# Kernel tuning notes

Measured on AMD Instinct MI355X. Metric: run time of the kernel, lower is better.

The kernel has to match this reference:

```python
import jax, jax.numpy as jnp
import numpy as np

N = 100000      # nodes
E = 1600000     # edges
F = 128         # num_node_features
H = 128         # hidden_channels
C = 10          # num_classes
R = 2           # num relations
G = 512         # num graphs in the batch


def setup_inputs() -> dict:
    key = jax.random.key(0)
    ks = jax.random.split(key, 16)
    s = 0.05
    x = jax.random.normal(ks[0], (N, F), dtype=jnp.float32)
    edge_index = jax.random.randint(ks[1], (2, E), 0, N, dtype=jnp.int64)
    edge_attr = jax.random.randint(ks[2], (E,), 0, R, dtype=jnp.int64)
    batch = jnp.sort(jax.random.randint(ks[3], (N,), 0, G, dtype=jnp.int64))
    W1 = jax.random.normal(ks[4], (R, F, H), dtype=jnp.float32) * s
    root1 = jax.random.normal(ks[5], (F, H), dtype=jnp.float32) * s
    b1 = jnp.zeros((H,), dtype=jnp.float32)
    W2 = jax.random.normal(ks[6], (R, H, H), dtype=jnp.float32) * s
    root2 = jax.random.normal(ks[7], (H, H), dtype=jnp.float32) * s
    b2 = jnp.zeros((H,), dtype=jnp.float32)
    W3 = jax.random.normal(ks[8], (R, H, H), dtype=jnp.float32) * s
    root3 = jax.random.normal(ks[9], (H, H), dtype=jnp.float32) * s
    b3 = jnp.zeros((H,), dtype=jnp.float32)
    lin_w = jax.random.normal(ks[10], (H, C), dtype=jnp.float32) * s
    lin_b = jnp.zeros((C,), dtype=jnp.float32)
    return dict(x=x, edge_index=edge_index, edge_attr=edge_attr, batch=batch,
                W1=W1, root1=root1, b1=b1, W2=W2, root2=root2, b2=b2,
                W3=W3, root3=root3, b3=b3, lin_w=lin_w, lin_b=lin_b)


def _rgcn_layer(x, src, dst, edge_type, W, root, b):
    # PyG RGCNConv: out = x @ root + b + sum_r mean_{edges of rel r -> i}(x_j @ W_r)
    n = x.shape[0]
    out = x @ root + b
    for r in range(R):
        h = x @ W[r]                               # [N, H] transform-then-gather
        w = (edge_type == r).astype(x.dtype)       # [E] relation mask
        num = jax.ops.segment_sum(h[src] * w[:, None], dst, num_segments=n)
        cnt = jax.ops.segment_sum(w, dst, num_segments=n)
        out = out + num / jnp.maximum(cnt, 1.0)[:, None]
    return out


def reference(x, edge_index, edge_attr, batch, W1, root1, b1, W2, root2, b2,
              W3, root3, b3, lin_w, lin_b):
    src, dst = edge_index[0], edge_index[1]
    h = jax.nn.relu(_rgcn_layer(x, src, dst, edge_attr, W1, root1, b1))
    h = jax.nn.relu(_rgcn_layer(h, src, dst, edge_attr, W2, root2, b2))
    h = jax.nn.relu(_rgcn_layer(h, src, dst, edge_attr, W3, root3, b3))
    # global mean pool over graphs
    psum = jax.ops.segment_sum(h, batch, num_segments=G)
    pcnt = jax.ops.segment_sum(jnp.ones((h.shape[0],), h.dtype), batch, num_segments=G)
    pooled = psum / jnp.maximum(pcnt, 1.0)[:, None]
    return pooled @ lin_w + lin_b
```

## Files before the change

kernel.cpp:

```cpp
#include <hip/hip_runtime.h>
#include <hip/hip_bf16.h>

#define Nn 100000
#define Ee 1600000
#define Ff 128
#define Hh 128
#define Cc 10
#define Gg 512

#define NBK 391
#define ABLK 4096
#define NABLK ((Ee + ABLK - 1) / ABLK)
#define BMAX 5376

typedef short bf16x8 __attribute__((ext_vector_type(8)));
typedef float f32x4 __attribute__((ext_vector_type(4)));
typedef float f32x2 __attribute__((ext_vector_type(2)));

__device__ __forceinline__ unsigned short f2bf(float f) {
    unsigned u = __float_as_uint(f);
    u += 0x7fffu + ((u >> 16) & 1u);
    return (unsigned short)(u >> 16);
}
__device__ __forceinline__ unsigned pk2(float a, float b) {
    return (unsigned)f2bf(a) | ((unsigned)f2bf(b) << 16);
}

__global__ __launch_bounds__(256) void cast_x(const float* __restrict__ x,
                                              uint2* __restrict__ xb) {
    int i = blockIdx.x * 256 + threadIdx.x;
    if (i >= Nn * Ff / 4) return;
    float4 v = ((const float4*)x)[i];
    uint2 o;
    o.x = pk2(v.x, v.y);
    o.y = pk2(v.z, v.w);
    xb[i] = o;
}

__global__ __launch_bounds__(256) void pack_w(const float* __restrict__ W1, const float* __restrict__ r1,
                                              const float* __restrict__ W2, const float* __restrict__ r2,
                                              const float* __restrict__ W3, const float* __restrict__ r3,
                                              unsigned short* __restrict__ wp) {
    int t = blockIdx.x * 256 + threadIdx.x;
    if (t >= 9 * 16384) return;
    int i = t & 7, l = (t >> 3) & 63, s = (t >> 9) & 3, c = (t >> 11) & 7, m = t >> 14;
    int k = s * 32 + ((l >> 4) << 3) + i;
    int n = (c << 4) + (l & 15);
    int q = m / 3, j = m % 3;
    const float* Ws[3] = {W1, W2, W3};
    const float* rs[3] = {r1, r2, r3};
    const float* src = (j == 0) ? rs[q] : (Ws[q] + (size_t)(j - 1) * Ff * Hh);
    wp[t] = f2bf(src[k * Hh + n]);
}

__global__ __launch_bounds__(512) void bin_edges(const int* __restrict__ ei,
                                                 const int* __restrict__ ea,
                                                 int* __restrict__ bucketCur,
                                                 int* __restrict__ csr) {
    __shared__ int lcnt[512];
    __shared__ int lstart[512];
    __shared__ int gbase[512];
    __shared__ int lcur[512];
    __shared__ int stage[ABLK];
    __shared__ unsigned short sbkt[ABLK];
    int t = threadIdx.x;
    int base = blockIdx.x * ABLK;
    int nhere = min(ABLK, Ee - base);
    lcnt[t] = 0;
    __syncthreads();
    for (int j = t; j < nhere; j += 512)
        atomicAdd(&lcnt[ei[Ee + base + j] >> 8], 1);
    __syncthreads();
    int v = lcnt[t];
    if (t < NBK) gbase[t] = (v > 0) ? atomicAdd(&bucketCur[t], v) : 0;
    int* pa = lcnt; int* pb = lstart;
    for (int off = 1; off < 512; off <<= 1) {
        int x = pa[t] + ((t >= off) ? pa[t - off] : 0);
        __syncthreads();
        pb[t] = x;
        __syncthreads();
        int* tmp = pa; pa = pb; pb = tmp;
    }
    int excl = pa[t] - v;
    __syncthreads();
    lstart[t] = excl;
    lcur[t] = excl;
    __syncthreads();
    for (int j = t; j < nhere; j += 512) {
        int e = base + j;
        int d = ei[Ee + e];
        int srcv = ei[e];
        int r = ea[e] & 1;
        int bkt = d >> 8;
        int lp = atomicAdd(&lcur[bkt], 1);
        stage[lp] = (srcv << 9) | ((d & 255) << 1) | r;
        sbkt[lp] = (unsigned short)bkt;
    }
    __syncthreads();
    for (int j = t; j < nhere; j += 512) {
        int bkt = sbkt[j];
        csr[(size_t)bkt * BMAX + gbase[bkt] + (j - lstart[bkt])] = stage[j];
    }
}

__global__ __launch_bounds__(512) void sort_bucket(const int* __restrict__ bucketCur,
                                                   int* __restrict__ csr,
                                                   int* __restrict__ rowstart,
                                                   int* __restrict__ mid,
                                                   int* __restrict__ rowend) {
    __shared__ int cnt_[512];
    __shared__ int start_[512];
    __shared__ int cur_[512];
    __shared__ int stage[BMAX];
    int b = blockIdx.x;
    int t = threadIdx.x;
    int s = b * BMAX;
    int n = bucketCur[b];
    cnt_[t] = 0;
    __syncthreads();
    for (int j = t; j < n; j += 512)
        atomicAdd(&cnt_[csr[(size_t)s + j] & 511], 1);
    __syncthreads();
    int v = cnt_[t];
    int* pa = cnt_; int* pb = start_;
    for (int off = 1; off < 512; off <<= 1) {
        int x = pa[t] + ((t >= off) ? pa[t - off] : 0);
        __syncthreads();
        pb[t] = x;
        __syncthreads();
        int* tmp = pa; pa = pb; pb = tmp;
    }
    int excl = pa[t] - v;
    __syncthreads();
    start_[t] = excl;
    cur_[t] = excl;
    __syncthreads();
    if (t < 256) {
        int d = b * 256 + t;
        if (d < Nn) {
            rowstart[d] = s + start_[2 * t];
            mid[d]      = s + start_[2 * t + 1];
            rowend[d]   = s + ((t < 255) ? start_[2 * t + 2] : n);
        }
    }
    for (int j = t; j < n; j += 512) {
        int rec = csr[(size_t)s + j];
        int lp = atomicAdd(&cur_[rec & 511], 1);
        stage[lp] = rec >> 9;
    }
    __syncthreads();
    for (int j = t; j < n; j += 512)
        csr[(size_t)s + j] = stage[j];
}

__global__ __launch_bounds__(256) void graph_starts(const int* __restrict__ batch,
                                                    int* __restrict__ gstart) {
    int n = blockIdx.x * 256 + threadIdx.x;
    if (n > Nn) return;
    int bp = (n == 0) ? -1 : batch[n - 1];
    int bc = (n == Nn) ? Gg : batch[n];
    for (int g = bp + 1; g <= bc; ++g) gstart[g] = n;
}

__device__ __forceinline__ void accbf(f32x2 A[4], uint4 v) {
    A[0] += (f32x2){__uint_as_float(v.x << 16), __uint_as_float(v.x & 0xffff0000u)};
    A[1] += (f32x2){__uint_as_float(v.y << 16), __uint_as_float(v.y & 0xffff0000u)};
    A[2] += (f32x2){__uint_as_float(v.z << 16), __uint_as_float(v.z & 0xffff0000u)};
    A[3] += (f32x2){__uint_as_float(v.w << 16), __uint_as_float(v.w & 0xffff0000u)};
}

__global__ __launch_bounds__(256) void aggregate(const unsigned short* __restrict__ xb,
                                                 const unsigned short* __restrict__ zrow,
                                                 const int* __restrict__ csr,
                                                 const int* __restrict__ rowstart,
                                                 const int* __restrict__ mid,
                                                 const int* __restrict__ rowend,
                                                 unsigned int* __restrict__ xg0,
                                                 unsigned int* __restrict__ xg1) {
    int d = blockIdx.x * 4 + (threadIdx.x >> 6);
    if (d >= Nn) return;
    int lane = threadIdx.x & 63;
    int slot = lane >> 4;
    int c8 = (lane & 15) * 8;
    int s = rowstart[d], md = mid[d], e = rowend[d];

    f32x2 A0[4], A1[4];
    #pragma unroll
    for (int j = 0; j < 4; ++j) { A0[j] = (f32x2){0.f, 0.f}; A1[j] = (f32x2){0.f, 0.f}; }

    int n0 = md - s, n1 = e - md;
    int nq = (max(n0, n1) + 3) >> 2;
    int lim0 = max(md - 1, 0);
    int lim1 = max(e - 1, 0);
    const unsigned short* zp = zrow + c8;

    #pragma unroll 2
    for (int q = 0; q < nq; ++q) {
        int i0 = s + q * 4 + slot;
        int i1 = md + q * 4 + slot;
        int r0 = csr[min(i0, lim0)];
        int r1 = csr[min(i1, lim1)];
        const unsigned short* p0 = (i0 < md) ? (xb + (size_t)r0 * Hh + c8) : zp;
        const unsigned short* p1 = (i1 < e)  ? (xb + (size_t)r1 * Hh + c8) : zp;
        uint4 v0 = *(const uint4*)p0;
        uint4 v1 = *(const uint4*)p1;
        accbf(A0, v0);
        accbf(A1, v1);
    }

    #pragma unroll
    for (int j = 0; j < 4; ++j) {
        A0[j].x += __shfl_xor(A0[j].x, 16); A0[j].y += __shfl_xor(A0[j].y, 16);
        A0[j].x += __shfl_xor(A0[j].x, 32); A0[j].y += __shfl_xor(A0[j].y, 32);
        A1[j].x += __shfl_xor(A1[j].x, 16); A1[j].y += __shfl_xor(A1[j].y, 16);
        A1[j].x += __shfl_xor(A1[j].x, 32); A1[j].y += __shfl_xor(A1[j].y, 32);
    }

    if (slot == 0) {
        float i0 = 1.f / fmaxf((float)n0, 1.f);
        float i1 = 1.f / fmaxf((float)n1, 1.f);
        uint4 o0, o1;
        o0.x = pk2(A0[0].x * i0, A0[0].y * i0);
        o0.y = pk2(A0[1].x * i0, A0[1].y * i0);
        o0.z = pk2(A0[2].x * i0, A0[2].y * i0);
        o0.w = pk2(A0[3].x * i0, A0[3].y * i0);
        o1.x = pk2(A1[0].x * i1, A1[0].y * i1);
        o1.y = pk2(A1[1].x * i1, A1[1].y * i1);
        o1.z = pk2(A1[2].x * i1, A1[2].y * i1);
        o1.w = pk2(A1[3].x * i1, A1[3].y * i1);
        *(uint4*)(xg0 + (size_t)d * (Hh / 2) + (lane & 15) * 4) = o0;
        *(uint4*)(xg1 + (size_t)d * (Hh / 2) + (lane & 15) * 4) = o1;
    }
}

__global__ __launch_bounds__(512, 2) void gemm_fused(const unsigned short* __restrict__ x0,
                                                     const unsigned short* __restrict__ xg0,
                                                     const unsigned short* __restrict__ xg1,
                                                     const unsigned short* __restrict__ wl,
                                                     const float* __restrict__ bias,
                                                     unsigned short* __restrict__ out) {
    __shared__ unsigned short wlds[16384];
    int t = threadIdx.x;
    int w = t >> 6, lane = t & 63;
    int m = lane & 15, ksel = lane >> 4;
    int row0 = blockIdx.x * 256 + w * 32;

    const unsigned short* srcs[3] = {x0, xg0, xg1};
    f32x4 acc[2][8];
    #pragma unroll
    for (int rt = 0; rt < 2; ++rt)
        #pragma unroll
        for (int cb = 0; cb < 8; ++cb) acc[rt][cb] = (f32x4){0.f, 0.f, 0.f, 0.f};

    #pragma unroll
    for (int mat = 0; mat < 3; ++mat) {
        if (mat) __syncthreads();
        {
            const uint4* ws_ = (const uint4*)(wl + (size_t)mat * 16384);
            uint4* wd_ = (uint4*)wlds;
            #pragma unroll
            for (int c = 0; c < 4; ++c) wd_[c * 512 + t] = ws_[c * 512 + t];
        }
        bf16x8 a[2][4];
        #pragma unroll
        for (int rt = 0; rt < 2; ++rt) {
            int node = row0 + rt * 16 + m;
            const unsigned short* xr = srcs[mat] + (size_t)node * Ff;
            #pragma unroll
            for (int s = 0; s < 4; ++s) {
                if (node < Nn) {
                    a[rt][s] = *(const bf16x8*)(xr + s * 32 + ksel * 8);
                } else {
                    #pragma unroll
                    for (int q = 0; q < 8; ++q) a[rt][s][q] = 0;
                }
            }
        }
        __syncthreads();
        #pragma unroll
        for (int cb = 0; cb < 8; ++cb) {
            #pragma unroll
            for (int s = 0; s < 4; ++s) {
                bf16x8 bfr = *(const bf16x8*)(wlds + (size_t)(cb * 4 + s) * 512 + lane * 8);
                acc[0][cb] = __builtin_amdgcn_mfma_f32_16x16x32_bf16(a[0][s], bfr, acc[0][cb], 0, 0, 0);
                acc[1][cb] = __builtin_amdgcn_mfma_f32_16x16x32_bf16(a[1][s], bfr, acc[1][cb], 0, 0, 0);
            }
        }
    }

    bool ev = (lane & 1) == 0;
    int j0 = ev ? 0 : 2;

    #pragma unroll
    for (int cb = 0; cb < 8; ++cb) {
        int col = cb * 16 + m;
        float bv = bias[col];
        int colb = col & ~1;
        #pragma unroll
        for (int rt = 0; rt < 2; ++rt) {
            f32x4 ac = acc[rt][cb];
            float o[4], po[4];
            #pragma unroll
            for (int j = 0; j < 4; ++j) o[j] = fmaxf(ac[j] + bv, 0.f);
            #pragma unroll
            for (int j = 0; j < 4; ++j) po[j] = __shfl_xor(o[j], 1);
            unsigned pkw0 = ev ? ((unsigned)f2bf(o[j0])      | ((unsigned)f2bf(po[j0])      << 16))
                               : ((unsigned)f2bf(po[j0])     | ((unsigned)f2bf(o[j0])       << 16));
            unsigned pkw1 = ev ? ((unsigned)f2bf(o[j0 + 1])  | ((unsigned)f2bf(po[j0 + 1])  << 16))
                               : ((unsigned)f2bf(po[j0 + 1]) | ((unsigned)f2bf(o[j0 + 1])   << 16));
            int rbase = row0 + rt * 16 + ksel * 4;
            int rr0 = rbase + j0, rr1 = rbase + j0 + 1;
            if (rr0 < Nn) *(unsigned*)(out + (size_t)rr0 * Hh + colb) = pkw0;
            if (rr1 < Nn) *(unsigned*)(out + (size_t)rr1 * Hh + colb) = pkw1;
        }
    }
}

__global__ __launch_bounds__(512) void pool_linear(const unsigned int* __restrict__ xb,
                                                   const int* __restrict__ gstart,
                                                   const float* __restrict__ lin_w,
                                                   const float* __restrict__ lin_b,
                                                   float* __restrict__ out) {
    __shared__ float red[8][128];
    int g = blockIdx.x;
    int t = threadIdx.x;
    int w = t >> 6, lane = t & 63;
    int s = gstart[g], e = gstart[g + 1];

    float a0 = 0.f, a1 = 0.f;
    for (int n = s + w; n < e; n += 8) {
        unsigned u = xb[(size_t)n * (Hh / 2) + lane];
        a0 += __uint_as_float(u << 16);
        a1 += __uint_as_float(u & 0xffff0000u);
    }
    red[w][lane * 2]     = a0;
    red[w][lane * 2 + 1] = a1;
    __syncthreads();

    if (w == 0) {
        #pragma unroll
        for (int ww = 1; ww < 8; ++ww) {
            a0 += red[ww][lane * 2];
            a1 += red[ww][lane * 2 + 1];
        }
        float inv = 1.f / fmaxf((float)(e - s), 1.f);
        a0 *= inv; a1 *= inv;
        float p[Cc];
        int k0 = 2 * lane, k1 = 2 * lane + 1;
        #pragma unroll
        for (int c = 0; c < Cc; ++c)
            p[c] = a0 * lin_w[k0 * Cc + c] + a1 * lin_w[k1 * Cc + c];
        #pragma unroll
        for (int off = 32; off > 0; off >>= 1)
            #pragma unroll
            for (int c = 0; c < Cc; ++c)
                p[c] += __shfl_down(p[c], off, 64);
        if (lane == 0)
            #pragma unroll
            for (int c = 0; c < Cc; ++c) out[g * Cc + c] = p[c] + lin_b[c];
    }
}

static inline size_t alignup(size_t v) { return (v + 255) & ~(size_t)255; }

extern "C" void kernel_launch(void* const* d_in, const int* in_sizes, int n_in,
                              void* d_out, int out_size, void* d_ws, size_t ws_size,
                              hipStream_t stream) {
    const float* x     = (const float*)d_in[0];
    const int*   ei    = (const int*)d_in[1];
    const int*   ea    = (const int*)d_in[2];
    const int*   batch = (const int*)d_in[3];
    const float* W1 = (const float*)d_in[4];
    const float* r1 = (const float*)d_in[5];
    const float* b1 = (const float*)d_in[6];
    const float* W2 = (const float*)d_in[7];
    const float* r2 = (const float*)d_in[8];
    const float* b2 = (const float*)d_in[9];
    const float* W3 = (const float*)d_in[10];
    const float* r3 = (const float*)d_in[11];
    const float* b3 = (const float*)d_in[12];
    const float* lin_w = (const float*)d_in[13];
    const float* lin_b = (const float*)d_in[14];
    float* out = (float*)d_out;

    char* p = (char*)d_ws;
    unsigned short* xbA = (unsigned short*)p;  p += alignup((size_t)Nn * Hh * 2);
    unsigned short* xbB = (unsigned short*)p;  p += alignup((size_t)Nn * Hh * 2);
    unsigned short* xg0 = (unsigned short*)p;  p += alignup((size_t)Nn * Hh * 2);
    unsigned short* xg1 = (unsigned short*)p;  p += alignup((size_t)Nn * Hh * 2);
    unsigned short* zrow = (unsigned short*)p; p += alignup((size_t)Hh * 2);
    unsigned short* wp  = (unsigned short*)p;  p += alignup((size_t)9 * 16384 * 2);
    int* rowstart    = (int*)p;                p += alignup((size_t)Nn * 4);
    int* mid         = (int*)p;                p += alignup((size_t)Nn * 4);
    int* rowend      = (int*)p;                p += alignup((size_t)Nn * 4);
    int* csr         = (int*)p;                p += alignup((size_t)NBK * BMAX * 4);
    int* bucketCur   = (int*)p;                p += alignup((size_t)NBK * 4);
    int* gstart      = (int*)p;                p += alignup((size_t)(Gg + 1) * 4);

    hipMemsetAsync(bucketCur, 0, (size_t)NBK * 4, stream);
    hipMemsetAsync(zrow, 0, (size_t)Hh * 2, stream);

    cast_x<<<(Nn * Ff / 4 + 255) / 256, 256, 0, stream>>>(x, (uint2*)xbA);
    pack_w<<<(9 * 16384 + 255) / 256, 256, 0, stream>>>(W1, r1, W2, r2, W3, r3, wp);

    bin_edges<<<NABLK, 512, 0, stream>>>(ei, ea, bucketCur, csr);
    sort_bucket<<<NBK, 512, 0, stream>>>(bucketCur, csr, rowstart, mid, rowend);

    graph_starts<<<(Nn + 1 + 255) / 256, 256, 0, stream>>>(batch, gstart);

    int agg_grid = (Nn + 3) / 4;
    int gemm_grid = (Nn + 255) / 256;

    aggregate<<<agg_grid, 256, 0, stream>>>(xbA, zrow, csr, rowstart, mid, rowend, (unsigned int*)xg0, (unsigned int*)xg1);
    gemm_fused<<<gemm_grid, 512, 0, stream>>>(xbA, xg0, xg1, wp + 0 * 3 * 16384, b1, xbB);
    aggregate<<<agg_grid, 256, 0, stream>>>(xbB, zrow, csr, rowstart, mid, rowend, (unsigned int*)xg0, (unsigned int*)xg1);
    gemm_fused<<<gemm_grid, 512, 0, stream>>>(xbB, xg0, xg1, wp + 1 * 3 * 16384, b2, xbA);
    aggregate<<<agg_grid, 256, 0, stream>>>(xbA, zrow, csr, rowstart, mid, rowend, (unsigned int*)xg0, (unsigned int*)xg1);
    gemm_fused<<<gemm_grid, 512, 0, stream>>>(xbA, xg0, xg1, wp + 2 * 3 * 16384, b3, xbB);

    pool_linear<<<Gg, 512, 0, stream>>>((const unsigned int*)xbB, gstart, lin_w, lin_b, out);
}
```

Measured before the change: 355.7 us.

## Pad per-relation CSR segments to equal multiples of four with sentinel zero row

The bucket sort now pads both relation segments of each destination node to the same length, a multiple of four, and fills the padding with a sentinel index that points at an extra zero row appended to each feature buffer. The aggregate loop drops the per-iteration bounds clamps and pointer selects and loads indices directly. Edge counts are packed into one int for the mean normalization. This trades extra padded gathers of the zero row and a larger CSR buffer (BMAX raised) for a simpler, branch-free inner loop.

```diff
diff --git a/kernel.cpp b/kernel.cpp
--- a/kernel.cpp
+++ b/kernel.cpp
@@ -11,7 +11,7 @@
 #define NBK 391
 #define ABLK 4096
 #define NABLK ((Ee + ABLK - 1) / ABLK)
-#define BMAX 5376
+#define BMAX 6656
 
 typedef short bf16x8 __attribute__((ext_vector_type(8)));
 typedef float f32x4 __attribute__((ext_vector_type(4)));
@@ -107,11 +107,13 @@
                                                    int* __restrict__ csr,
                                                    int* __restrict__ rowstart,
                                                    int* __restrict__ mid,
-                                                   int* __restrict__ rowend) {
+                                                   int* __restrict__ cnts) {
     __shared__ int cnt_[512];
-    __shared__ int start_[512];
+    __shared__ int sa_[512];
+    __shared__ int sb_[512];
     __shared__ int cur_[512];
     __shared__ int stage[BMAX];
+    __shared__ int npad_s;
     int b = blockIdx.x;
     int t = threadIdx.x;
     int s = b * BMAX;
@@ -121,8 +123,13 @@
     for (int j = t; j < n; j += 512)
         atomicAdd(&cnt_[csr[(size_t)s + j] & 511], 1);
     __syncthreads();
-    int v = cnt_[t];
-    int* pa = cnt_; int* pb = start_;
+    int c_self = cnt_[t];
+    int c_pair = cnt_[t ^ 1];
+    int Lp = (max(c_self, c_pair) + 3) & ~3;
+    int v = Lp;
+    sa_[t] = v;
+    __syncthreads();
+    int* pa = sa_; int* pb = sb_;
     for (int off = 1; off < 512; off <<= 1) {
         int x = pa[t] + ((t >= off) ? pa[t - off] : 0);
         __syncthreads();
@@ -131,25 +138,29 @@
         int* tmp = pa; pa = pb; pb = tmp;
     }
     int excl = pa[t] - v;
-    __syncthreads();
-    start_[t] = excl;
+    if (t == 511) npad_s = excl + v;
+    __syncthreads();
+    sa_[t] = excl;
     cur_[t] = excl;
     __syncthreads();
+    int npad = npad_s;
     if (t < 256) {
         int d = b * 256 + t;
         if (d < Nn) {
-            rowstart[d] = s + start_[2 * t];
-            mid[d]      = s + start_[2 * t + 1];
-            rowend[d]   = s + ((t < 255) ? start_[2 * t + 2] : n);
-        }
-    }
+            rowstart[d] = s + sa_[2 * t];
+            mid[d]      = s + sa_[2 * t + 1];
+            cnts[d]     = cnt_[2 * t] | (cnt_[2 * t + 1] << 16);
+        }
+    }
+    for (int j = t; j < npad; j += 512) stage[j] = Nn;
+    __syncthreads();
     for (int j = t; j < n; j += 512) {
         int rec = csr[(size_t)s + j];
         int lp = atomicAdd(&cur_[rec & 511], 1);
         stage[lp] = rec >> 9;
     }
     __syncthreads();
-    for (int j = t; j < n; j += 512)
+    for (int j = t; j < npad; j += 512)
         csr[(size_t)s + j] = stage[j];
 }
 
@@ -170,11 +181,10 @@
 }
 
 __global__ __launch_bounds__(256) void aggregate(const unsigned short* __restrict__ xb,
-                                                 const unsigned short* __restrict__ zrow,
                                                  const int* __restrict__ csr,
                                                  const int* __restrict__ rowstart,
                                                  const int* __restrict__ mid,
-                                                 const int* __restrict__ rowend,
+                                                 const int* __restrict__ cnts,
                                                  unsigned int* __restrict__ xg0,
                                                  unsigned int* __restrict__ xg1) {
     int d = blockIdx.x * 4 + (threadIdx.x >> 6);
@@ -182,28 +192,22 @@
     int lane = threadIdx.x & 63;
     int slot = lane >> 4;
     int c8 = (lane & 15) * 8;
-    int s = rowstart[d], md = mid[d], e = rowend[d];
+    int s = rowstart[d], md = mid[d];
+    int nq = (md - s) >> 2;
 
     f32x2 A0[4], A1[4];
     #pragma unroll
     for (int j = 0; j < 4; ++j) { A0[j] = (f32x2){0.f, 0.f}; A1[j] = (f32x2){0.f, 0.f}; }
 
-    int n0 = md - s, n1 = e - md;
-    int nq = (max(n0, n1) + 3) >> 2;
-    int lim0 = max(md - 1, 0);
-    int lim1 = max(e - 1, 0);
-    const unsigned short* zp = zrow + c8;
+    const int* p0 = csr + s + slot;
+    const int* p1 = csr + md + slot;
 
     #pragma unroll 2
     for (int q = 0; q < nq; ++q) {
-        int i0 = s + q * 4 + slot;
-        int i1 = md + q * 4 + slot;
-        int r0 = csr[min(i0, lim0)];
-        int r1 = csr[min(i1, lim1)];
-        const unsigned short* p0 = (i0 < md) ? (xb + (size_t)r0 * Hh + c8) : zp;
-        const unsigned short* p1 = (i1 < e)  ? (xb + (size_t)r1 * Hh + c8) : zp;
-        uint4 v0 = *(const uint4*)p0;
-        uint4 v1 = *(const uint4*)p1;
+        int r0 = p0[q * 4];
+        int r1 = p1[q * 4];
+        uint4 v0 = *(const uint4*)(xb + (size_t)r0 * Hh + c8);
+        uint4 v1 = *(const uint4*)(xb + (size_t)r1 * Hh + c8);
         accbf(A0, v0);
         accbf(A1, v1);
     }
@@ -217,6 +221,8 @@
     }
 
     if (slot == 0) {
+        int cn = cnts[d];
+        int n0 = cn & 0xffff, n1 = cn >> 16;
         float i0 = 1.f / fmaxf((float)n0, 1.f);
         float i1 = 1.f / fmaxf((float)n1, 1.f);
         uint4 o0, o1;
@@ -384,38 +390,38 @@
     float* out = (float*)d_out;
 
     char* p = (char*)d_ws;
-    unsigned short* xbA = (unsigned short*)p;  p += alignup((size_t)Nn * Hh * 2);
-    unsigned short* xbB = (unsigned short*)p;  p += alignup((size_t)Nn * Hh * 2);
+    unsigned short* xbA = (unsigned short*)p;  p += alignup((size_t)(Nn + 1) * Hh * 2);
+    unsigned short* xbB = (unsigned short*)p;  p += alignup((size_t)(Nn + 1) * Hh * 2);
     unsigned short* xg0 = (unsigned short*)p;  p += alignup((size_t)Nn * Hh * 2);
     unsigned short* xg1 = (unsigned short*)p;  p += alignup((size_t)Nn * Hh * 2);
-    unsigned short* zrow = (unsigned short*)p; p += alignup((size_t)Hh * 2);
     unsigned short* wp  = (unsigned short*)p;  p += alignup((size_t)9 * 16384 * 2);
     int* rowstart    = (int*)p;                p += alignup((size_t)Nn * 4);
     int* mid         = (int*)p;                p += alignup((size_t)Nn * 4);
-    int* rowend      = (int*)p;                p += alignup((size_t)Nn * 4);
+    int* cnts        = (int*)p;                p += alignup((size_t)Nn * 4);
     int* csr         = (int*)p;                p += alignup((size_t)NBK * BMAX * 4);
     int* bucketCur   = (int*)p;                p += alignup((size_t)NBK * 4);
     int* gstart      = (int*)p;                p += alignup((size_t)(Gg + 1) * 4);
 
     hipMemsetAsync(bucketCur, 0, (size_t)NBK * 4, stream);
-    hipMemsetAsync(zrow, 0, (size_t)Hh * 2, stream);
+    hipMemsetAsync(xbA + (size_t)Nn * Hh, 0, Hh * 2, stream);
+    hipMemsetAsync(xbB + (size_t)Nn * Hh, 0, Hh * 2, stream);
 
     cast_x<<<(Nn * Ff / 4 + 255) / 256, 256, 0, stream>>>(x, (uint2*)xbA);
     pack_w<<<(9 * 16384 + 255) / 256, 256, 0, stream>>>(W1, r1, W2, r2, W3, r3, wp);
 
     bin_edges<<<NABLK, 512, 0, stream>>>(ei, ea, bucketCur, csr);
-    sort_bucket<<<NBK, 512, 0, stream>>>(bucketCur, csr, rowstart, mid, rowend);
+    sort_bucket<<<NBK, 512, 0, stream>>>(bucketCur, csr, rowstart, mid, cnts);
 
     graph_starts<<<(Nn + 1 + 255) / 256, 256, 0, stream>>>(batch, gstart);
 
     int agg_grid = (Nn + 3) / 4;
     int gemm_grid = (Nn + 255) / 256;
 
-    aggregate<<<agg_grid, 256, 0, stream>>>(xbA, zrow, csr, rowstart, mid, rowend, (unsigned int*)xg0, (unsigned int*)xg1);
+    aggregate<<<agg_grid, 256, 0, stream>>>(xbA, csr, rowstart, mid, cnts, (unsigned int*)xg0, (unsigned int*)xg1);
     gemm_fused<<<gemm_grid, 512, 0, stream>>>(xbA, xg0, xg1, wp + 0 * 3 * 16384, b1, xbB);
-    aggregate<<<agg_grid, 256, 0, stream>>>(xbB, zrow, csr, rowstart, mid, rowend, (unsigned int*)xg0, (unsigned int*)xg1);
+    aggregate<<<agg_grid, 256, 0, stream>>>(xbB, csr, rowstart, mid, cnts, (unsigned int*)xg0, (unsigned int*)xg1);
     gemm_fused<<<gemm_grid, 512, 0, stream>>>(xbB, xg0, xg1, wp + 1 * 3 * 16384, b2, xbA);
-    aggregate<<<agg_grid, 256, 0, stream>>>(xbA, zrow, csr, rowstart, mid, rowend, (unsigned int*)xg0, (unsigned int*)xg1);
+    aggregate<<<agg_grid, 256, 0, stream>>>(xbA, csr, rowstart, mid, cnts, (unsigned int*)xg0, (unsigned int*)xg1);
     gemm_fused<<<gemm_grid, 512, 0, stream>>>(xbA, xg0, xg1, wp + 2 * 3 * 16384, b3, xbB);
 
     pool_linear<<<Gg, 512, 0, stream>>>((const unsigned int*)xbB, gstart, lin_w, lin_b, out);
```

Result: no change. 359.4 us, median of 3 (+1.1%).
